# Optimization experiments

Hardware: AMD Instinct MI355X
Metric: run time of the kernel (lower is better)

## Reference

```python
import jax, jax.numpy as jnp
import numpy as np

B, C_IN, H, W = 4, 512, 188, 188
SHARED_CH = 64
NUM_CLASS = 3
M = 200
NUM_MAX = 500
STRIDE = 8
PCR = (-75.2, -75.2, -2.0, 75.2, 75.2, 4.0)
VOX = (0.1, 0.1, 0.15)
OUT_CH = (2, 1, 3, 2, 1, 3)  # center, center_z, dim, rot, iou, hm
MIN_RADIUS = 2.0
OVERLAP = 0.1
INIT_BIAS = -2.19


def conv3x3(x, w):
    return jax.lax.conv_general_dilated(x, w, (1, 1), 'SAME',
                                        dimension_numbers=('NCHW', 'OIHW', 'NCHW'))


def bn_relu(x, p):
    # p: [4, C] = gamma, beta, running_mean, running_var (inference-mode BN)
    g, b, m, v = p[0], p[1], p[2], p[3]
    scale = (g * jax.lax.rsqrt(v + 1e-5))[None, :, None, None]
    y = (x - m[None, :, None, None]) * scale + b[None, :, None, None]
    return jax.nn.relu(y)


def gaussian_radius(height, width, min_overlap):
    # Faithful to OpenPCDet centernet_utils.gaussian_radius
    b1 = height + width
    c1 = width * height * (1 - min_overlap) / (1 + min_overlap)
    sq1 = jnp.sqrt(jnp.maximum(b1 * b1 - 4.0 * c1, 0.0))
    r1 = (b1 + sq1) / 2.0
    b2 = 2.0 * (height + width)
    c2 = (1 - min_overlap) * width * height
    sq2 = jnp.sqrt(jnp.maximum(b2 * b2 - 16.0 * c2, 0.0))
    r2 = (b2 + sq2) / 2.0
    a3 = 4.0 * min_overlap
    b3 = -2.0 * min_overlap * (height + width)
    c3 = (min_overlap - 1.0) * width * height
    sq3 = jnp.sqrt(jnp.maximum(b3 * b3 - 4.0 * a3 * c3, 0.0))
    r3 = (b3 + sq3) / 2.0
    return jnp.minimum(jnp.minimum(r1, r2), r3)


def assign_targets(gt_boxes):
    # gt_boxes: [B, M, 8] = x, y, z, dx, dy, dz, heading, class(1..NUM_CLASS)
    x, y, z = gt_boxes[..., 0], gt_boxes[..., 1], gt_boxes[..., 2]
    dx, dy, dz = gt_boxes[..., 3], gt_boxes[..., 4], gt_boxes[..., 5]
    heading = gt_boxes[..., 6]
    cls = jax.lax.stop_gradient(gt_boxes[..., 7]).astype(jnp.int32)

    cx = jnp.clip((x - PCR[0]) / VOX[0] / STRIDE, 0.0, W - 0.5)  # [B,M]
    cy = jnp.clip((y - PCR[1]) / VOX[1] / STRIDE, 0.0, H - 0.5)
    cxi = jax.lax.stop_gradient(jnp.floor(cx)).astype(jnp.int32)  # .int() trunc == floor (>=0)
    cyi = jax.lax.stop_gradient(jnp.floor(cy)).astype(jnp.int32)

    dxp = dx / VOX[0] / STRIDE
    dyp = dy / VOX[1] / STRIDE
    r = gaussian_radius(dxp, dyp, OVERLAP)
    r = jnp.maximum(jnp.floor(jax.lax.stop_gradient(r)), MIN_RADIUS)  # clamp_min(r.int(), 2)
    sigma = (2.0 * r + 1.0) / 6.0
    valid = (dx > 0) & (dy > 0)  # [B,M]

    ox = jnp.arange(W, dtype=jnp.int32)[None, None, :] - cxi[..., None]  # [B,M,W]
    oy = jnp.arange(H, dtype=jnp.int32)[None, None, :] - cyi[..., None]  # [B,M,H]
    d2 = (oy.astype(jnp.float32) ** 2)[:, :, :, None] + (ox.astype(jnp.float32) ** 2)[:, :, None, :]
    g = jnp.exp(-d2 / (2.0 * sigma * sigma)[:, :, None, None])  # [B,M,H,W]
    win = (jnp.abs(oy)[:, :, :, None] <= r[:, :, None, None]) & \
          (jnp.abs(ox)[:, :, None, :] <= r[:, :, None, None])
    g = jnp.where(win & valid[:, :, None, None], g, 0.0)

    # per-class max-splat (draw_gaussian_to_heatmap uses torch.max overlap)
    heatmap = jnp.stack(
        [jnp.max(jnp.where((cls == c + 1)[:, :, None, None], g, 0.0), axis=1)
         for c in range(NUM_CLASS)], axis=1)  # [B,NUM_CLASS,H,W]

    vf = valid.astype(gt_boxes.dtype)
    vals = jnp.stack([cx - cxi.astype(cx.dtype), cy - cyi.astype(cy.dtype), z,
                      jnp.log(dx), jnp.log(dy), jnp.log(dz),
                      jnp.cos(heading), jnp.sin(heading)], axis=-1) * vf[..., None]
    target_boxes = jnp.zeros((B, NUM_MAX, 8), gt_boxes.dtype).at[:, :M].set(vals)
    ind_vals = (cyi * W + cxi) * valid.astype(jnp.int32)
    inds = jnp.zeros((B, NUM_MAX), jnp.int32).at[:, :M].set(ind_vals)
    mask = jnp.zeros((B, NUM_MAX), jnp.int32).at[:, :M].set(valid.astype(jnp.int32))
    return heatmap, target_boxes, inds, mask


def setup_inputs() -> dict:
    key = jax.random.key(0)
    ks = jax.random.split(key, 16)
    spatial_features = jax.random.normal(ks[0], (B, C_IN, H, W), jnp.float32)
    x = jax.random.uniform(ks[1], (B, M), minval=-70.0, maxval=70.0)
    y = jax.random.uniform(ks[2], (B, M), minval=-70.0, maxval=70.0)
    z = jax.random.uniform(ks[3], (B, M), minval=-1.0, maxval=1.0)
    dx = jax.random.uniform(ks[4], (B, M), minval=1.5, maxval=5.0)
    dy = jax.random.uniform(ks[5], (B, M), minval=1.5, maxval=5.0)
    dz = jax.random.uniform(ks[6], (B, M), minval=1.0, maxval=3.0)
    hd = jax.random.uniform(ks[7], (B, M), minval=-np.pi, maxval=np.pi)
    cls = jax.random.randint(ks[8], (B, M), 1, NUM_CLASS + 1).astype(jnp.float32)
    gt_boxes = jnp.stack([x, y, z, dx, dy, dz, hd, cls], axis=-1)

    def mk_bn(k, lead):
        kk = jax.random.split(k, 4)
        g = 1.0 + 0.1 * jax.random.normal(kk[0], lead + (SHARED_CH,))
        b = 0.1 * jax.random.normal(kk[1], lead + (SHARED_CH,))
        m = 0.1 * jax.random.normal(kk[2], lead + (SHARED_CH,))
        v = jax.random.uniform(kk[3], lead + (SHARED_CH,), minval=0.5, maxval=1.5)
        return jnp.stack([g, b, m, v], axis=len(lead))

    w_shared = jax.random.normal(ks[9], (SHARED_CH, C_IN, 3, 3)) * (1.0 / np.sqrt(C_IN * 9))
    bn_shared = mk_bn(ks[10], ())
    w1_heads = jax.random.normal(ks[11], (6, SHARED_CH, SHARED_CH, 3, 3)) * (1.0 / np.sqrt(SHARED_CH * 9))
    bn_heads = mk_bn(ks[12], (6,))
    w2_heads = jax.random.normal(ks[13], (6, 3, SHARED_CH, 3, 3)) * (1.0 / np.sqrt(SHARED_CH * 9))
    b2_heads = jnp.zeros((6, 3), jnp.float32).at[5].set(INIT_BIAS)  # hm branch bias = -2.19
    return {'spatial_features': spatial_features, 'gt_boxes': gt_boxes,
            'w_shared': w_shared, 'bn_shared': bn_shared,
            'w1_heads': w1_heads, 'bn_heads': bn_heads,
            'w2_heads': w2_heads, 'b2_heads': b2_heads}


def reference(spatial_features, gt_boxes, w_shared, bn_shared,
              w1_heads, bn_heads, w2_heads, b2_heads):
    shared = bn_relu(conv3x3(spatial_features, w_shared), bn_shared)  # [B,64,H,W]

    def branch(w1, bnp, w2, b2):
        h = bn_relu(conv3x3(shared, w1), bnp)
        return conv3x3(h, w2) + b2[None, :, None, None]  # [B,3,H,W] (out padded to 3)

    outs = jax.vmap(branch)(w1_heads, bn_heads, w2_heads, b2_heads)  # [6,B,3,H,W]
    head_out = jnp.concatenate([outs[i, :, :OUT_CH[i]] for i in range(6)], axis=1)  # [B,12,H,W]

    heatmap, target_boxes, inds, mask = assign_targets(gt_boxes)
    return head_out, heatmap, target_boxes, inds, mask
```

## Files before the change

### kernel.cpp

```cpp
#include <hip/hip_runtime.h>
#include <hip/hip_bf16.h>

#define HWD 188
#define NPX (HWD*HWD)
#define NB 4
#define CIN 512
#define CH 64
#define MBOX 200
#define NMAX 500

#define HEAD_SZ (NB*12*NPX)
#define HM_OFF  HEAD_SZ
#define TB_OFF  (HM_OFF + NB*3*NPX)
#define IND_OFF (TB_OFF + NB*NMAX*8)
#define MSK_OFF (IND_OFF + NB*NMAX)

typedef short sh8 __attribute__((ext_vector_type(8)));
typedef float f4 __attribute__((ext_vector_type(4)));
typedef unsigned short us4 __attribute__((ext_vector_type(4)));

__device__ __constant__ int d_cum[6]  = {0, 2, 3, 6, 8, 9};
__device__ __constant__ int d_outc[6] = {2, 1, 3, 2, 1, 3};

__device__ __forceinline__ unsigned short bf16_bits(float v) {
  union { __hip_bfloat16 h; unsigned short u; } cv;
  cv.h = __float2bfloat16(v);
  return cv.u;
}

__global__ __launch_bounds__(256) void wprep(
    const float* __restrict__ ws_, const float* __restrict__ w1_,
    const float* __restrict__ w2_, unsigned short* __restrict__ w1b,
    unsigned short* __restrict__ w2b, unsigned short* __restrict__ w3b) {
  int e = blockIdx.x * 256 + threadIdx.x;
  const int N1 = 9 * 64 * 512;
  const int N2 = 6 * 9 * 64 * 64;
  const int N3 = 6 * 9 * 16 * 64;
  if (e < N1) {
    int tap = e / (64 * 512); int r = e % (64 * 512);
    int oc = r / 512; int ic = r % 512;
    w1b[e] = bf16_bits(ws_[(oc * 512 + ic) * 9 + tap]);
  } else if (e < N1 + N2) {
    int f = e - N1;
    int h = f / (9 * 64 * 64); int r = f % (9 * 64 * 64);
    int tap = r / (64 * 64); int r2 = r % (64 * 64);
    int oc = r2 / 64; int ic = r2 % 64;
    w2b[f] = bf16_bits(w1_[((h * 64 + oc) * 64 + ic) * 9 + tap]);
  } else if (e < N1 + N2 + N3) {
    int f = e - N1 - N2;
    int h = f / (9 * 16 * 64); int r = f % (9 * 16 * 64);
    int tap = r / (16 * 64); int r2 = r % (16 * 64);
    int oc = r2 / 64; int ic = r2 % 64;
    float v = (oc < 3) ? w2_[((h * 3 + oc) * 64 + ic) * 9 + tap] : 0.f;
    w3b[f] = bf16_bits(v);
  }
}

__global__ __launch_bounds__(256) void conv1_mfma(
    const float* __restrict__ sf,
    const unsigned short* __restrict__ wb,
    const float* __restrict__ bnp,
    unsigned short* __restrict__ outp) {
  __shared__ __align__(16) short s_in[10 * 34 * 32];
  const int t = threadIdx.x;
  const int b = blockIdx.y;
  const int rt = blockIdx.x / 6, ct = blockIdx.x % 6;
  const int y0 = rt * 8, x0 = ct * 32;
  const int w = t >> 6, lane = t & 63, ln = lane & 15, kg = lane >> 4;

  f4 acc[4][4];
#pragma unroll
  for (int i = 0; i < 4; ++i)
#pragma unroll
    for (int j = 0; j < 4; ++j) acc[i][j] = (f4){0.f, 0.f, 0.f, 0.f};

  for (int ic0 = 0; ic0 < CIN; ic0 += 32) {
    __syncthreads();
    for (int idx = t; idx < 2720; idx += 256) {
      int c = idx % 34; int rem = idx / 34;
      int r = rem % 10; int iq = rem / 10;
      int gy = y0 - 1 + r, gx = x0 - 1 + c;
      float v0 = 0.f, v1 = 0.f, v2 = 0.f, v3 = 0.f;
      if (gy >= 0 && gy < HWD && gx >= 0 && gx < HWD) {
        const float* p = sf + ((b * CIN + ic0 + iq * 4) * HWD + gy) * HWD + gx;
        v0 = p[0]; v1 = p[NPX]; v2 = p[2 * NPX]; v3 = p[3 * NPX];
      }
      us4 pk = {bf16_bits(v0), bf16_bits(v1), bf16_bits(v2), bf16_bits(v3)};
      *reinterpret_cast<us4*>(&s_in[(r * 34 + c) * 32 + iq * 4]) = pk;
    }
    __syncthreads();
    for (int tap = 0; tap < 9; ++tap) {
      const int ky = tap / 3, kx = tap % 3;
      sh8 af[4];
#pragma unroll
      for (int ot = 0; ot < 4; ++ot)
        af[ot] = *reinterpret_cast<const sh8*>(
            wb + (tap * 64 + ot * 16 + ln) * CIN + ic0 + kg * 8);
#pragma unroll
      for (int nt = 0; nt < 4; ++nt) {
        const int rr = 2 * w + (nt >> 1) + ky;
        const int cc = (nt & 1) * 16 + ln + kx;
        sh8 bf = *reinterpret_cast<const sh8*>(&s_in[(rr * 34 + cc) * 32 + kg * 8]);
#pragma unroll
        for (int ot = 0; ot < 4; ++ot)
          acc[ot][nt] = __builtin_amdgcn_mfma_f32_16x16x32_bf16(
              af[ot], bf, acc[ot][nt], 0, 0, 0);
      }
    }
  }
#pragma unroll
  for (int ot = 0; ot < 4; ++ot) {
    const int ocb = ot * 16 + kg * 4;
    f4 g4 = *reinterpret_cast<const f4*>(bnp + ocb);
    f4 b4 = *reinterpret_cast<const f4*>(bnp + 64 + ocb);
    f4 m4 = *reinterpret_cast<const f4*>(bnp + 128 + ocb);
    f4 v4 = *reinterpret_cast<const f4*>(bnp + 192 + ocb);
    f4 sc, bi;
#pragma unroll
    for (int j = 0; j < 4; ++j) {
      sc[j] = g4[j] * rsqrtf(v4[j] + 1e-5f);
      bi[j] = b4[j] - m4[j] * sc[j];
    }
#pragma unroll
    for (int nt = 0; nt < 4; ++nt) {
      int y = y0 + 2 * w + (nt >> 1);
      int x = x0 + (nt & 1) * 16 + ln;
      if (y < HWD && x < HWD) {
        us4 pk;
#pragma unroll
        for (int j = 0; j < 4; ++j)
          pk[j] = bf16_bits(fmaxf(acc[ot][nt][j] * sc[j] + bi[j], 0.f));
        *reinterpret_cast<us4*>(outp + ((b * HWD + y) * HWD + x) * 64 + ocb) = pk;
      }
    }
  }
}

template<int OCT, int EPI>
__global__ __launch_bounds__(256) void conv_head_mfma(
    const unsigned short* __restrict__ inp,
    const unsigned short* __restrict__ wb0,
    const float* __restrict__ bn0,
    const float* __restrict__ b2,
    unsigned short* __restrict__ outp0,
    float* __restrict__ hout,
    int h_base, long long stride) {
  __shared__ __align__(16) short s_in[10 * 34 * 32];
  const int t = threadIdx.x;
  const int b = blockIdx.y;
  const int h = h_base + blockIdx.z;
  const int rt = blockIdx.x / 6, ct = blockIdx.x % 6;
  const int y0 = rt * 8, x0 = ct * 32;
  const int w = t >> 6, lane = t & 63, ln = lane & 15, kg = lane >> 4;

  const unsigned short* wb = wb0 + h * (9 * OCT * 16 * 64);
  const unsigned short* in_t = (EPI == 1) ? inp + h * stride : inp;

  f4 acc[OCT][4];
#pragma unroll
  for (int i = 0; i < OCT; ++i)
#pragma unroll
    for (int j = 0; j < 4; ++j) acc[i][j] = (f4){0.f, 0.f, 0.f, 0.f};

  for (int ic0 = 0; ic0 < CH; ic0 += 32) {
    __syncthreads();
    for (int idx = t; idx < 1360; idx += 256) {
      int icg = idx & 3; int pix = idx >> 2;
      int c = pix % 34; int r = pix / 34;
      int gy = y0 - 1 + r, gx = x0 - 1 + c;
      sh8 v = (sh8){0, 0, 0, 0, 0, 0, 0, 0};
      if (gy >= 0 && gy < HWD && gx >= 0 && gx < HWD)
        v = *reinterpret_cast<const sh8*>(
            &in_t[((b * HWD + gy) * HWD + gx) * 64 + ic0 + icg * 8]);
      *reinterpret_cast<sh8*>(&s_in[(r * 34 + c) * 32 + icg * 8]) = v;
    }
    __syncthreads();
    for (int tap = 0; tap < 9; ++tap) {
      const int ky = tap / 3, kx = tap % 3;
      sh8 af[OCT];
#pragma unroll
      for (int ot = 0; ot < OCT; ++ot)
        af[ot] = *reinterpret_cast<const sh8*>(
            wb + (tap * OCT * 16 + ot * 16 + ln) * 64 + ic0 + kg * 8);
#pragma unroll
      for (int nt = 0; nt < 4; ++nt) {
        const int rr = 2 * w + (nt >> 1) + ky;
        const int cc = (nt & 1) * 16 + ln + kx;
        sh8 bf = *reinterpret_cast<const sh8*>(&s_in[(rr * 34 + cc) * 32 + kg * 8]);
#pragma unroll
        for (int ot = 0; ot < OCT; ++ot)
          acc[ot][nt] = __builtin_amdgcn_mfma_f32_16x16x32_bf16(
              af[ot], bf, acc[ot][nt], 0, 0, 0);
      }
    }
  }
  if (EPI == 0) {
    unsigned short* outp = outp0 + h * stride;
#pragma unroll
    for (int ot = 0; ot < OCT; ++ot) {
      const int ocb = ot * 16 + kg * 4;
      const float* bnp = bn0 + h * 256;
      f4 g4 = *reinterpret_cast<const f4*>(bnp + ocb);
      f4 b4 = *reinterpret_cast<const f4*>(bnp + 64 + ocb);
      f4 m4 = *reinterpret_cast<const f4*>(bnp + 128 + ocb);
      f4 v4 = *reinterpret_cast<const f4*>(bnp + 192 + ocb);
      f4 sc, bi;
#pragma unroll
      for (int j = 0; j < 4; ++j) {
        sc[j] = g4[j] * rsqrtf(v4[j] + 1e-5f);
        bi[j] = b4[j] - m4[j] * sc[j];
      }
#pragma unroll
      for (int nt = 0; nt < 4; ++nt) {
        int y = y0 + 2 * w + (nt >> 1);
        int x = x0 + (nt & 1) * 16 + ln;
        if (y < HWD && x < HWD) {
          us4 pk;
#pragma unroll
          for (int j = 0; j < 4; ++j)
            pk[j] = bf16_bits(fmaxf(acc[ot][nt][j] * sc[j] + bi[j], 0.f));
          *reinterpret_cast<us4*>(outp + ((b * HWD + y) * HWD + x) * 64 + ocb) = pk;
        }
      }
    }
  } else {
    const int c_off = d_cum[h], noc = d_outc[h];
    const float* bias = b2 + h * 3;
#pragma unroll
    for (int nt = 0; nt < 4; ++nt) {
      int y = y0 + 2 * w + (nt >> 1);
      int x = x0 + (nt & 1) * 16 + ln;
      if (y < HWD && x < HWD) {
#pragma unroll
        for (int j = 0; j < 4; ++j) {
          int oc = kg * 4 + j;
          if (oc < noc)
            hout[(b * 12 + c_off + oc) * NPX + y * HWD + x] =
                acc[0][nt][j] + bias[oc];
        }
      }
    }
  }
}

__global__ __launch_bounds__(256) void targets_kernel(
    const float* __restrict__ gt, float* __restrict__ out, float* __restrict__ boxp) {
  int idx = blockIdx.x * 256 + threadIdx.x;
  if (idx >= NB * NMAX) return;
  int b = idx / NMAX, j = idx - b * NMAX;
  float vals[8] = {0, 0, 0, 0, 0, 0, 0, 0};
  float indf = 0.f, mkf = 0.f;
  if (j < MBOX) {
    const float* g = gt + (b * MBOX + j) * 8;
    float x = g[0], y = g[1], z = g[2], dx = g[3], dy = g[4], dz = g[5];
    float hd = g[6], cls = g[7];
    float cx = (x - (-75.2f)) / 0.1f / 8.0f;
    cx = fminf(fmaxf(cx, 0.0f), (float)HWD - 0.5f);
    float cy = (y - (-75.2f)) / 0.1f / 8.0f;
    cy = fminf(fmaxf(cy, 0.0f), (float)HWD - 0.5f);
    float cxf = floorf(cx), cyf = floorf(cy);
    int cxi = (int)cxf, cyi = (int)cyf;
    float hh = dx / 0.1f / 8.0f;
    float ww = dy / 0.1f / 8.0f;
    const float ov = 0.1f;
    float b1 = hh + ww;
    float c1 = ww * hh * (1.0f - ov) / (1.0f + ov);
    float sq1 = sqrtf(fmaxf(b1 * b1 - 4.0f * c1, 0.0f));
    float r1 = (b1 + sq1) / 2.0f;
    float b2_ = 2.0f * (hh + ww);
    float c2 = (1.0f - ov) * ww * hh;
    float sq2 = sqrtf(fmaxf(b2_ * b2_ - 16.0f * c2, 0.0f));
    float r2 = (b2_ + sq2) / 2.0f;
    float a3 = 4.0f * ov;
    float b3 = -2.0f * ov * (hh + ww);
    float c3 = (ov - 1.0f) * ww * hh;
    float sq3 = sqrtf(fmaxf(b3 * b3 - 4.0f * a3 * c3, 0.0f));
    float r3 = (b3 + sq3) / 2.0f;
    float r = fminf(fminf(r1, r2), r3);
    r = fmaxf(floorf(r), 2.0f);
    float sigma = (2.0f * r + 1.0f) / 6.0f;
    float inv2s2 = 1.0f / (2.0f * sigma * sigma);
    bool valid = (dx > 0.0f) && (dy > 0.0f);
    float vf = valid ? 1.0f : 0.0f;
    vals[0] = (cx - cxf) * vf;
    vals[1] = (cy - cyf) * vf;
    vals[2] = z * vf;
    vals[3] = logf(dx) * vf;
    vals[4] = logf(dy) * vf;
    vals[5] = logf(dz) * vf;
    vals[6] = cosf(hd) * vf;
    vals[7] = sinf(hd) * vf;
    indf = (float)((cyi * HWD + cxi) * (valid ? 1 : 0));
    mkf = vf;
    float* bp = boxp + (b * MBOX + j) * 8;
    bp[0] = cxf; bp[1] = cyf; bp[2] = r; bp[3] = inv2s2;
    bp[4] = valid ? cls : 0.0f; bp[5] = 0.f; bp[6] = 0.f; bp[7] = 0.f;
  }
  float* tb = out + TB_OFF + (b * NMAX + j) * 8;
#pragma unroll
  for (int k = 0; k < 8; ++k) tb[k] = vals[k];
  out[IND_OFF + b * NMAX + j] = indf;
  out[MSK_OFF + b * NMAX + j] = mkf;
}

__global__ __launch_bounds__(256) void heatmap_kernel(
    const float* __restrict__ boxp, float* __restrict__ out) {
  __shared__ float s_bp[MBOX][5];
  const int t = threadIdx.x, b = blockIdx.y;
  for (int e = t; e < MBOX * 5; e += 256) {
    int j = e / 5, k = e - j * 5;
    s_bp[j][k] = boxp[(b * MBOX + j) * 8 + k];
  }
  __syncthreads();
  int p = blockIdx.x * 256 + t;
  if (p >= NPX) return;
  int y = p / HWD, x = p - y * HWD;
  float a0 = 0.f, a1 = 0.f, a2 = 0.f;
  for (int j = 0; j < MBOX; ++j) {
    int c = (int)s_bp[j][4];
    if (c == 0) continue;
    float ox = (float)x - s_bp[j][0];
    float oy = (float)y - s_bp[j][1];
    float r = s_bp[j][2];
    if (fabsf(ox) <= r && fabsf(oy) <= r) {
      float gg = expf(-(ox * ox + oy * oy) * s_bp[j][3]);
      if (c == 1) a0 = fmaxf(a0, gg);
      else if (c == 2) a1 = fmaxf(a1, gg);
      else a2 = fmaxf(a2, gg);
    }
  }
  int base = HM_OFF + (b * 3 * HWD + y) * HWD + x;
  out[base] = a0;
  out[base + NPX] = a1;
  out[base + 2 * NPX] = a2;
}

extern "C" void kernel_launch(void* const* d_in, const int* in_sizes, int n_in,
                              void* d_out, int out_size, void* d_ws, size_t ws_size,
                              hipStream_t stream) {
  (void)in_sizes; (void)n_in; (void)out_size;
  const float* sf = (const float*)d_in[0];
  const float* gt = (const float*)d_in[1];
  const float* w_shared = (const float*)d_in[2];
  const float* bn_shared = (const float*)d_in[3];
  const float* w1 = (const float*)d_in[4];
  const float* bnH = (const float*)d_in[5];
  const float* w2 = (const float*)d_in[6];
  const float* b2 = (const float*)d_in[7];
  float* out = (float*)d_out;
  char* ws = (char*)d_ws;

  const size_t SH = (size_t)NB * NPX * 64 * 2;
  unsigned short* shared_t = (unsigned short*)ws;
  unsigned short* w1b = (unsigned short*)(ws + SH);
  unsigned short* w2b = (unsigned short*)(ws + SH + 589824);
  unsigned short* w3b = (unsigned short*)(ws + SH + 589824 + 442368);
  float* boxp = (float*)(ws + SH + 589824 + 442368 + 110592);
  unsigned short* tmp0 = (unsigned short*)(ws + SH + 589824 + 442368 + 110592 + 25600);

  const size_t need_wide = SH + 589824 + 442368 + 110592 + 25600 + 6 * SH;
  const bool wide = ws_size >= need_wide;
  const long long tstride = wide ? (long long)(SH / 2) : 0LL;

  wprep<<<2232, 256, 0, stream>>>(w_shared, w1, w2, w1b, w2b, w3b);
  conv1_mfma<<<dim3(144, NB), 256, 0, stream>>>(sf, w1b, bn_shared, shared_t);

  if (wide) {
    conv_head_mfma<4, 0><<<dim3(144, NB, 6), 256, 0, stream>>>(
        shared_t, w2b, bnH, nullptr, tmp0, nullptr, 0, tstride);
    conv_head_mfma<1, 1><<<dim3(144, NB, 6), 256, 0, stream>>>(
        tmp0, w3b, nullptr, b2, nullptr, out, 0, tstride);
  } else {
    for (int h = 0; h < 6; ++h) {
      conv_head_mfma<4, 0><<<dim3(144, NB), 256, 0, stream>>>(
          shared_t, w2b, bnH, nullptr, tmp0, nullptr, h, 0);
      conv_head_mfma<1, 1><<<dim3(144, NB), 256, 0, stream>>>(
          tmp0, w3b, nullptr, b2, nullptr, out, h, 0);
    }
  }

  targets_kernel<<<(NB * NMAX + 255) / 256, 256, 0, stream>>>(gt, out, boxp);
  heatmap_kernel<<<dim3((NPX + 255) / 256, NB), 256, 0, stream>>>(boxp, out);
}
```

Before: 664.6 us.

## Restructure conv kernels: double-buffered conv1, shared-tile multi-head conv2, XCD swizzle

Measured after the change: 686.6 us. 3.3% more time.

```diff
diff --git a/kernel.cpp b/kernel.cpp
--- a/kernel.cpp
+++ b/kernel.cpp
@@ -28,18 +28,23 @@
   return cv.u;
 }
 
+__device__ __forceinline__ int xcd_swz(int bid, int grid) {
+  return (bid & 7) * (grid >> 3) + (bid >> 3);
+}
+
 __global__ __launch_bounds__(256) void wprep(
     const float* __restrict__ ws_, const float* __restrict__ w1_,
     const float* __restrict__ w2_, unsigned short* __restrict__ w1b,
     unsigned short* __restrict__ w2b, unsigned short* __restrict__ w3b) {
   int e = blockIdx.x * 256 + threadIdx.x;
-  const int N1 = 9 * 64 * 512;
+  const int N1 = 9 * 16 * 64 * 32;
   const int N2 = 6 * 9 * 64 * 64;
   const int N3 = 6 * 9 * 16 * 64;
   if (e < N1) {
-    int tap = e / (64 * 512); int r = e % (64 * 512);
-    int oc = r / 512; int ic = r % 512;
-    w1b[e] = bf16_bits(ws_[(oc * 512 + ic) * 9 + tap]);
+    int icr = e & 31; int r1 = e >> 5;
+    int oc = r1 & 63; int r2 = r1 >> 6;
+    int icq = r2 & 15; int tap = r2 >> 4;
+    w1b[e] = bf16_bits(ws_[(oc * 512 + icq * 32 + icr) * 9 + tap]);
   } else if (e < N1 + N2) {
     int f = e - N1;
     int h = f / (9 * 64 * 64); int r = f % (9 * 64 * 64);
@@ -56,61 +61,114 @@
   }
 }
 
-__global__ __launch_bounds__(256) void conv1_mfma(
+#define C1_LDS (10*18*32)
+__global__ __launch_bounds__(256, 4) void conv1_mfma(
     const float* __restrict__ sf,
     const unsigned short* __restrict__ wb,
     const float* __restrict__ bnp,
     unsigned short* __restrict__ outp) {
-  __shared__ __align__(16) short s_in[10 * 34 * 32];
+  __shared__ __align__(16) short s_in[2][C1_LDS];
   const int t = threadIdx.x;
-  const int b = blockIdx.y;
-  const int rt = blockIdx.x / 6, ct = blockIdx.x % 6;
-  const int y0 = rt * 8, x0 = ct * 32;
+  const int swz = xcd_swz(blockIdx.x, 1152);
+  const int b = swz / 288;
+  const int tt = swz % 288;
+  const int y0 = (tt / 12) * 8, x0 = (tt % 12) * 16;
   const int w = t >> 6, lane = t & 63, ln = lane & 15, kg = lane >> 4;
-
-  f4 acc[4][4];
-#pragma unroll
-  for (int i = 0; i < 4; ++i)
+  const int rg = w & 1, og = w >> 1;
+
+  const bool st_act = (t < 240);
+  const int icg = t & 3, cg = (t >> 2) % 6, sr = (t >> 2) / 6;
+  const int gy_s = y0 - 1 + sr;
+  const int gx0_s = x0 - 4 + cg * 4;
+  const bool row_ok = (gy_s >= 0 && gy_s < HWD);
+  const bool vec_ok = (gx0_s >= 0 && gx0_s + 3 < HWD);
+  const float* sbase = sf + (((long long)b * CIN + icg * 8) * HWD + gy_s) * HWD + gx0_s;
+
+  f4 acc[2][4];
+#pragma unroll
+  for (int i = 0; i < 2; ++i)
 #pragma unroll
     for (int j = 0; j < 4; ++j) acc[i][j] = (f4){0.f, 0.f, 0.f, 0.f};
 
-  for (int ic0 = 0; ic0 < CIN; ic0 += 32) {
-    __syncthreads();
-    for (int idx = t; idx < 2720; idx += 256) {
-      int c = idx % 34; int rem = idx / 34;
-      int r = rem % 10; int iq = rem / 10;
-      int gy = y0 - 1 + r, gx = x0 - 1 + c;
-      float v0 = 0.f, v1 = 0.f, v2 = 0.f, v3 = 0.f;
-      if (gy >= 0 && gy < HWD && gx >= 0 && gx < HWD) {
-        const float* p = sf + ((b * CIN + ic0 + iq * 4) * HWD + gy) * HWD + gx;
-        v0 = p[0]; v1 = p[NPX]; v2 = p[2 * NPX]; v3 = p[3 * NPX];
-      }
-      us4 pk = {bf16_bits(v0), bf16_bits(v1), bf16_bits(v2), bf16_bits(v3)};
-      *reinterpret_cast<us4*>(&s_in[(r * 34 + c) * 32 + iq * 4]) = pk;
-    }
-    __syncthreads();
+  f4 st[8];
+#pragma unroll
+  for (int j = 0; j < 8; ++j) st[j] = (f4){0.f, 0.f, 0.f, 0.f};
+
+#define C1_LOAD(IC0)                                                        \
+  do {                                                                      \
+    if (st_act && row_ok) {                                                 \
+      const float* p = sbase + (long long)(IC0) * NPX;                      \
+      if (vec_ok) {                                                         \
+        _Pragma("unroll")                                                   \
+        for (int j = 0; j < 8; ++j)                                         \
+          st[j] = *reinterpret_cast<const f4*>(p + (long long)j * NPX);     \
+      } else {                                                              \
+        _Pragma("unroll")                                                   \
+        for (int j = 0; j < 8; ++j) st[j] = (f4){0.f, 0.f, 0.f, 0.f};       \
+        _Pragma("unroll")                                                   \
+        for (int k = 0; k < 4; ++k) {                                       \
+          int gx = gx0_s + k;                                               \
+          if (gx >= 0 && gx < HWD) {                                        \
+            _Pragma("unroll")                                               \
+            for (int j = 0; j < 8; ++j) st[j][k] = p[(long long)j * NPX + k];\
+          }                                                                 \
+        }                                                                   \
+      }                                                                     \
+    } else {                                                                \
+      _Pragma("unroll")                                                     \
+      for (int j = 0; j < 8; ++j) st[j] = (f4){0.f, 0.f, 0.f, 0.f};         \
+    }                                                                       \
+  } while (0)
+
+#define C1_WRITE(BUF)                                                       \
+  do {                                                                      \
+    if (st_act) {                                                           \
+      _Pragma("unroll")                                                     \
+      for (int k = 0; k < 4; ++k) {                                         \
+        int col = cg * 4 + k - 3;                                           \
+        if ((unsigned)col < 18u) {                                          \
+          sh8 pk;                                                           \
+          _Pragma("unroll")                                                 \
+          for (int j = 0; j < 8; ++j) pk[j] = (short)bf16_bits(st[j][k]);   \
+          *reinterpret_cast<sh8*>(&(BUF)[(sr * 18 + col) * 32 + icg * 8]) = pk; \
+        }                                                                   \
+      }                                                                     \
+    }                                                                       \
+  } while (0)
+
+  C1_LOAD(0);
+  C1_WRITE(s_in[0]);
+  __syncthreads();
+
+  for (int s = 0; s < 16; ++s) {
+    const short* cur = s_in[s & 1];
+    if (s < 15) C1_LOAD((s + 1) * 32);
+#pragma unroll
     for (int tap = 0; tap < 9; ++tap) {
       const int ky = tap / 3, kx = tap % 3;
-      sh8 af[4];
-#pragma unroll
-      for (int ot = 0; ot < 4; ++ot)
-        af[ot] = *reinterpret_cast<const sh8*>(
-            wb + (tap * 64 + ot * 16 + ln) * CIN + ic0 + kg * 8);
+      sh8 af[2];
+#pragma unroll
+      for (int i = 0; i < 2; ++i)
+        af[i] = *reinterpret_cast<const sh8*>(
+            wb + (((tap * 16 + s) * 64) + (2 * og + i) * 16 + ln) * 32 + kg * 8);
 #pragma unroll
       for (int nt = 0; nt < 4; ++nt) {
-        const int rr = 2 * w + (nt >> 1) + ky;
-        const int cc = (nt & 1) * 16 + ln + kx;
-        sh8 bf = *reinterpret_cast<const sh8*>(&s_in[(rr * 34 + cc) * 32 + kg * 8]);
-#pragma unroll
-        for (int ot = 0; ot < 4; ++ot)
-          acc[ot][nt] = __builtin_amdgcn_mfma_f32_16x16x32_bf16(
-              af[ot], bf, acc[ot][nt], 0, 0, 0);
-      }
-    }
-  }
-#pragma unroll
-  for (int ot = 0; ot < 4; ++ot) {
-    const int ocb = ot * 16 + kg * 4;
+        const int rr = 4 * rg + nt + ky;
+        const int cc = ln + kx;
+        sh8 bf = *reinterpret_cast<const sh8*>(&cur[(rr * 18 + cc) * 32 + kg * 8]);
+#pragma unroll
+        for (int i = 0; i < 2; ++i)
+          acc[i][nt] = __builtin_amdgcn_mfma_f32_16x16x32_bf16(
+              af[i], bf, acc[i][nt], 0, 0, 0);
+      }
+    }
+    if (s < 15) C1_WRITE(s_in[(s & 1) ^ 1]);
+    __syncthreads();
+  }
+
+#pragma unroll
+  for (int i = 0; i < 2; ++i) {
+    const int ocb = (2 * og + i) * 16 + kg * 4;
     f4 g4 = *reinterpret_cast<const f4*>(bnp + ocb);
     f4 b4 = *reinterpret_cast<const f4*>(bnp + 64 + ocb);
     f4 m4 = *reinterpret_cast<const f4*>(bnp + 128 + ocb);
@@ -123,83 +181,81 @@
     }
 #pragma unroll
     for (int nt = 0; nt < 4; ++nt) {
-      int y = y0 + 2 * w + (nt >> 1);
-      int x = x0 + (nt & 1) * 16 + ln;
+      int y = y0 + 4 * rg + nt;
+      int x = x0 + ln;
       if (y < HWD && x < HWD) {
         us4 pk;
 #pragma unroll
         for (int j = 0; j < 4; ++j)
-          pk[j] = bf16_bits(fmaxf(acc[ot][nt][j] * sc[j] + bi[j], 0.f));
-        *reinterpret_cast<us4*>(outp + ((b * HWD + y) * HWD + x) * 64 + ocb) = pk;
-      }
-    }
-  }
-}
-
-template<int OCT, int EPI>
-__global__ __launch_bounds__(256) void conv_head_mfma(
+          pk[j] = bf16_bits(fmaxf(acc[i][nt][j] * sc[j] + bi[j], 0.f));
+        *reinterpret_cast<us4*>(outp + (((long long)b * HWD + y) * HWD + x) * 64 + ocb) = pk;
+      }
+    }
+  }
+#undef C1_LOAD
+#undef C1_WRITE
+}
+
+__global__ __launch_bounds__(256, 3) void conv2_allheads(
     const unsigned short* __restrict__ inp,
-    const unsigned short* __restrict__ wb0,
-    const float* __restrict__ bn0,
-    const float* __restrict__ b2,
-    unsigned short* __restrict__ outp0,
-    float* __restrict__ hout,
-    int h_base, long long stride) {
-  __shared__ __align__(16) short s_in[10 * 34 * 32];
+    const unsigned short* __restrict__ w2b,
+    const float* __restrict__ bnH,
+    unsigned short* __restrict__ tmp0,
+    int h_lo, int h_hi, long long tstride) {
+  __shared__ __align__(16) short s_in[10 * 34 * 72];
   const int t = threadIdx.x;
-  const int b = blockIdx.y;
-  const int h = h_base + blockIdx.z;
-  const int rt = blockIdx.x / 6, ct = blockIdx.x % 6;
-  const int y0 = rt * 8, x0 = ct * 32;
+  const int swz = xcd_swz(blockIdx.x, gridDim.x);
+  const int b = swz / 144;
+  const int tt = swz % 144;
+  const int y0 = (tt / 6) * 8, x0 = (tt % 6) * 32;
   const int w = t >> 6, lane = t & 63, ln = lane & 15, kg = lane >> 4;
 
-  const unsigned short* wb = wb0 + h * (9 * OCT * 16 * 64);
-  const unsigned short* in_t = (EPI == 1) ? inp + h * stride : inp;
-
-  f4 acc[OCT][4];
-#pragma unroll
-  for (int i = 0; i < OCT; ++i)
-#pragma unroll
-    for (int j = 0; j < 4; ++j) acc[i][j] = (f4){0.f, 0.f, 0.f, 0.f};
-
-  for (int ic0 = 0; ic0 < CH; ic0 += 32) {
-    __syncthreads();
-    for (int idx = t; idx < 1360; idx += 256) {
-      int icg = idx & 3; int pix = idx >> 2;
-      int c = pix % 34; int r = pix / 34;
-      int gy = y0 - 1 + r, gx = x0 - 1 + c;
-      sh8 v = (sh8){0, 0, 0, 0, 0, 0, 0, 0};
-      if (gy >= 0 && gy < HWD && gx >= 0 && gx < HWD)
-        v = *reinterpret_cast<const sh8*>(
-            &in_t[((b * HWD + gy) * HWD + gx) * 64 + ic0 + icg * 8]);
-      *reinterpret_cast<sh8*>(&s_in[(r * 34 + c) * 32 + icg * 8]) = v;
-    }
-    __syncthreads();
-    for (int tap = 0; tap < 9; ++tap) {
-      const int ky = tap / 3, kx = tap % 3;
-      sh8 af[OCT];
-#pragma unroll
-      for (int ot = 0; ot < OCT; ++ot)
-        af[ot] = *reinterpret_cast<const sh8*>(
-            wb + (tap * OCT * 16 + ot * 16 + ln) * 64 + ic0 + kg * 8);
-#pragma unroll
-      for (int nt = 0; nt < 4; ++nt) {
-        const int rr = 2 * w + (nt >> 1) + ky;
-        const int cc = (nt & 1) * 16 + ln + kx;
-        sh8 bf = *reinterpret_cast<const sh8*>(&s_in[(rr * 34 + cc) * 32 + kg * 8]);
-#pragma unroll
-        for (int ot = 0; ot < OCT; ++ot)
-          acc[ot][nt] = __builtin_amdgcn_mfma_f32_16x16x32_bf16(
-              af[ot], bf, acc[ot][nt], 0, 0, 0);
-      }
-    }
-  }
-  if (EPI == 0) {
-    unsigned short* outp = outp0 + h * stride;
-#pragma unroll
-    for (int ot = 0; ot < OCT; ++ot) {
+  for (int idx = t; idx < 2720; idx += 256) {
+    int ch = idx & 7; int pix = idx >> 3;
+    int c = pix % 34; int r = pix / 34;
+    int gy = y0 - 1 + r, gx = x0 - 1 + c;
+    sh8 v = (sh8){0, 0, 0, 0, 0, 0, 0, 0};
+    if (gy >= 0 && gy < HWD && gx >= 0 && gx < HWD)
+      v = *reinterpret_cast<const sh8*>(
+          &inp[(((long long)b * HWD + gy) * HWD + gx) * 64 + ch * 8]);
+    *reinterpret_cast<sh8*>(&s_in[(r * 34 + c) * 72 + ch * 8]) = v;
+  }
+  __syncthreads();
+
+  for (int h = h_lo; h < h_hi; ++h) {
+    f4 acc[4][4];
+#pragma unroll
+    for (int i = 0; i < 4; ++i)
+#pragma unroll
+      for (int j = 0; j < 4; ++j) acc[i][j] = (f4){0.f, 0.f, 0.f, 0.f};
+#pragma unroll
+    for (int icq = 0; icq < 2; ++icq) {
+#pragma unroll
+      for (int tap = 0; tap < 9; ++tap) {
+        const int ky = tap / 3, kx = tap % 3;
+        sh8 af[4];
+#pragma unroll
+        for (int ot = 0; ot < 4; ++ot)
+          af[ot] = *reinterpret_cast<const sh8*>(
+              w2b + (((h * 9 + tap) * 64) + ot * 16 + ln) * 64 + icq * 32 + kg * 8);
+#pragma unroll
+        for (int nt = 0; nt < 4; ++nt) {
+          const int rr = 2 * w + (nt >> 1) + ky;
+          const int cc = (nt & 1) * 16 + ln + kx;
+          sh8 bf = *reinterpret_cast<const sh8*>(
+              &s_in[(rr * 34 + cc) * 72 + icq * 32 + kg * 8]);
+#pragma unroll
+          for (int ot = 0; ot < 4; ++ot)
+            acc[ot][nt] = __builtin_amdgcn_mfma_f32_16x16x32_bf16(
+                af[ot], bf, acc[ot][nt], 0, 0, 0);
+        }
+      }
+    }
+    unsigned short* outp = tmp0 + (long long)h * tstride;
+    const float* bnp = bnH + h * 256;
+#pragma unroll
+    for (int ot = 0; ot < 4; ++ot) {
       const int ocb = ot * 16 + kg * 4;
-      const float* bnp = bn0 + h * 256;
       f4 g4 = *reinterpret_cast<const f4*>(bnp + ocb);
       f4 b4 = *reinterpret_cast<const f4*>(bnp + 64 + ocb);
       f4 m4 = *reinterpret_cast<const f4*>(bnp + 128 + ocb);
@@ -219,25 +275,74 @@
 #pragma unroll
           for (int j = 0; j < 4; ++j)
             pk[j] = bf16_bits(fmaxf(acc[ot][nt][j] * sc[j] + bi[j], 0.f));
-          *reinterpret_cast<us4*>(outp + ((b * HWD + y) * HWD + x) * 64 + ocb) = pk;
+          *reinterpret_cast<us4*>(outp + (((long long)b * HWD + y) * HWD + x) * 64 + ocb) = pk;
         }
       }
     }
-  } else {
-    const int c_off = d_cum[h], noc = d_outc[h];
-    const float* bias = b2 + h * 3;
-#pragma unroll
-    for (int nt = 0; nt < 4; ++nt) {
-      int y = y0 + 2 * w + (nt >> 1);
-      int x = x0 + (nt & 1) * 16 + ln;
-      if (y < HWD && x < HWD) {
-#pragma unroll
-        for (int j = 0; j < 4; ++j) {
-          int oc = kg * 4 + j;
-          if (oc < noc)
-            hout[(b * 12 + c_off + oc) * NPX + y * HWD + x] =
-                acc[0][nt][j] + bias[oc];
-        }
+  }
+}
+
+__global__ __launch_bounds__(256, 3) void conv3_mfma(
+    const unsigned short* __restrict__ tmp0,
+    const unsigned short* __restrict__ w3b,
+    const float* __restrict__ b2,
+    float* __restrict__ hout,
+    int h_base, long long tstride) {
+  __shared__ __align__(16) short s_in[10 * 34 * 72];
+  const int t = threadIdx.x;
+  const int swz = xcd_swz(blockIdx.x, gridDim.x);
+  const int h = h_base + swz / 576;
+  const int rem = swz % 576;
+  const int b = rem / 144;
+  const int tt = rem % 144;
+  const int y0 = (tt / 6) * 8, x0 = (tt % 6) * 32;
+  const int w = t >> 6, lane = t & 63, ln = lane & 15, kg = lane >> 4;
+  const unsigned short* inp = tmp0 + (long long)h * tstride;
+
+  for (int idx = t; idx < 2720; idx += 256) {
+    int ch = idx & 7; int pix = idx >> 3;
+    int c = pix % 34; int r = pix / 34;
+    int gy = y0 - 1 + r, gx = x0 - 1 + c;
+    sh8 v = (sh8){0, 0, 0, 0, 0, 0, 0, 0};
+    if (gy >= 0 && gy < HWD && gx >= 0 && gx < HWD)
+      v = *reinterpret_cast<const sh8*>(
+          &inp[(((long long)b * HWD + gy) * HWD + gx) * 64 + ch * 8]);
+    *reinterpret_cast<sh8*>(&s_in[(r * 34 + c) * 72 + ch * 8]) = v;
+  }
+  __syncthreads();
+
+  f4 acc[4];
+#pragma unroll
+  for (int j = 0; j < 4; ++j) acc[j] = (f4){0.f, 0.f, 0.f, 0.f};
+#pragma unroll
+  for (int icq = 0; icq < 2; ++icq) {
+#pragma unroll
+    for (int tap = 0; tap < 9; ++tap) {
+      const int ky = tap / 3, kx = tap % 3;
+      sh8 af = *reinterpret_cast<const sh8*>(
+          w3b + (((h * 9 + tap) * 16) + ln) * 64 + icq * 32 + kg * 8);
+#pragma unroll
+      for (int nt = 0; nt < 4; ++nt) {
+        const int rr = 2 * w + (nt >> 1) + ky;
+        const int cc = (nt & 1) * 16 + ln + kx;
+        sh8 bf = *reinterpret_cast<const sh8*>(
+            &s_in[(rr * 34 + cc) * 72 + icq * 32 + kg * 8]);
+        acc[nt] = __builtin_amdgcn_mfma_f32_16x16x32_bf16(af, bf, acc[nt], 0, 0, 0);
+      }
+    }
+  }
+  const int c_off = d_cum[h], noc = d_outc[h];
+#pragma unroll
+  for (int nt = 0; nt < 4; ++nt) {
+    int y = y0 + 2 * w + (nt >> 1);
+    int x = x0 + (nt & 1) * 16 + ln;
+    if (y < HWD && x < HWD) {
+#pragma unroll
+      for (int j = 0; j < 4; ++j) {
+        int oc = kg * 4 + j;
+        if (oc < noc)
+          hout[((long long)b * 12 + c_off + oc) * NPX + y * HWD + x] =
+              acc[nt][j] + b2[h * 3 + oc];
       }
     }
   }
@@ -356,26 +461,23 @@
   unsigned short* w2b = (unsigned short*)(ws + SH + 589824);
   unsigned short* w3b = (unsigned short*)(ws + SH + 589824 + 442368);
   float* boxp = (float*)(ws + SH + 589824 + 442368 + 110592);
-  unsigned short* tmp0 = (unsigned short*)(ws + SH + 589824 + 442368 + 110592 + 25600);
-
-  const size_t need_wide = SH + 589824 + 442368 + 110592 + 25600 + 6 * SH;
-  const bool wide = ws_size >= need_wide;
+  const size_t off_tmp = SH + 589824 + 442368 + 110592 + 25600;
+  unsigned short* tmp0 = (unsigned short*)(ws + off_tmp);
+
+  const bool wide = ws_size >= off_tmp + 6 * SH;
   const long long tstride = wide ? (long long)(SH / 2) : 0LL;
 
   wprep<<<2232, 256, 0, stream>>>(w_shared, w1, w2, w1b, w2b, w3b);
-  conv1_mfma<<<dim3(144, NB), 256, 0, stream>>>(sf, w1b, bn_shared, shared_t);
+
+  conv1_mfma<<<1152, 256, 0, stream>>>(sf, w1b, bn_shared, shared_t);
 
   if (wide) {
-    conv_head_mfma<4, 0><<<dim3(144, NB, 6), 256, 0, stream>>>(
-        shared_t, w2b, bnH, nullptr, tmp0, nullptr, 0, tstride);
-    conv_head_mfma<1, 1><<<dim3(144, NB, 6), 256, 0, stream>>>(
-        tmp0, w3b, nullptr, b2, nullptr, out, 0, tstride);
+    conv2_allheads<<<576, 256, 0, stream>>>(shared_t, w2b, bnH, tmp0, 0, 6, tstride);
+    conv3_mfma<<<3456, 256, 0, stream>>>(tmp0, w3b, b2, out, 0, tstride);
   } else {
     for (int h = 0; h < 6; ++h) {
-      conv_head_mfma<4, 0><<<dim3(144, NB), 256, 0, stream>>>(
-          shared_t, w2b, bnH, nullptr, tmp0, nullptr, h, 0);
-      conv_head_mfma<1, 1><<<dim3(144, NB), 256, 0, stream>>>(
-          tmp0, w3b, nullptr, b2, nullptr, out, h, 0);
+      conv2_allheads<<<576, 256, 0, stream>>>(shared_t, w2b, bnH, tmp0, h, h + 1, 0);
+      conv3_mfma<<<576, 256, 0, stream>>>(tmp0, w3b, b2, out, h, 0);
     }
   }
 
```
